# Optimization experiments

Hardware: AMD Instinct MI355X
Metric: run time of the kernel (lower is better)

The kernel has to match this reference:

```python
import jax, jax.numpy as jnp
import numpy as np

B, S, D, R = 8, 2048, 2048, 4  # batch, seq, dim, n_roles


def setup_inputs() -> dict:
    key = jax.random.key(0)
    k1, k2, k3 = jax.random.split(key, 3)
    hidden = jax.random.normal(k1, (B, S, D), dtype=jnp.float32)
    roles = jax.random.randint(k2, (B,), 0, R)
    role_onehot = jax.nn.one_hot(roles, R, dtype=jnp.float32)  # [B, R]
    # per-role Linear params (nn.Linear(dim, dim)), Kaiming-ish init scale
    W = jax.random.normal(k3, (R, D, D), dtype=jnp.float32) / np.sqrt(D)
    b = jnp.zeros((R, D), dtype=jnp.float32)
    scales = jnp.ones((R,), dtype=jnp.float32)  # role_scales
    return {"hidden": hidden, "role_onehot": role_onehot, "W": W, "b": b, "scales": scales}


def reference(hidden, role_onehot, W, b, scales):
    # Training path: compute every role's Linear+Tanh*scale, then mask-sum by one-hot.
    # transformed: [R, B, S, D]
    t = jnp.tanh(jnp.einsum('bsd,rde->rbse', hidden, W) + b[:, None, None, :])
    t = t * scales[:, None, None, None]
    # weights = role_onehot^T broadcast over (S, D); sum over roles
    return jnp.einsum('rbse,br->bse', t, role_onehot)
```

## Files before the change

kernel.cpp:

```cpp
#include <hip/hip_runtime.h>
#include <stdint.h>


#define BDIM 8
#define SDIM 2048
#define DDIM 2048
#define RDIM 4

typedef __attribute__((ext_vector_type(8))) short bf16x8;
typedef __attribute__((ext_vector_type(4))) float f32x4;

typedef unsigned int uint32;
typedef unsigned short ushort16_t;

__device__ __forceinline__ unsigned short f2bf(float f) {
    uint32 u = __float_as_uint(f);
    u += 0x7fffu + ((u >> 16) & 1u);
    return (unsigned short)(u >> 16);
}
__device__ __forceinline__ uint32 pack2(float lo, float hi) {
    return (uint32)f2bf(lo) | ((uint32)f2bf(hi) << 16);
}


__global__ __launch_bounds__(256) void cvt_h_kernel(const float* __restrict__ h,
                                                    unsigned short* __restrict__ o, int n4) {
    int i = blockIdx.x * blockDim.x + threadIdx.x;
    int stride = gridDim.x * blockDim.x;
    for (; i < n4; i += stride) {
        float4 v = reinterpret_cast<const float4*>(h)[i];
        uint2 p;
        p.x = pack2(v.x, v.y);
        p.y = pack2(v.z, v.w);
        reinterpret_cast<uint2*>(o)[i] = p;
    }
}

__global__ __launch_bounds__(256) void cvt_wt_kernel(const float* __restrict__ w,
                                                     unsigned short* __restrict__ o) {
    __shared__ unsigned short tile[32][33];
    int r = blockIdx.z;
    int e0 = blockIdx.x * 32, d0 = blockIdx.y * 32;
    const float* wr = w + (size_t)r * DDIM * DDIM;
    unsigned short* orr = o + (size_t)r * DDIM * DDIM;
    #pragma unroll
    for (int i = threadIdx.y; i < 32; i += 8)
        tile[i][threadIdx.x] = f2bf(wr[(size_t)(d0 + i) * DDIM + e0 + threadIdx.x]);
    __syncthreads();
    #pragma unroll
    for (int i = threadIdx.y; i < 32; i += 8)
        orr[(size_t)(e0 + i) * DDIM + d0 + threadIdx.x] = tile[threadIdx.x][i];
}


template <bool PRE>
__global__ __launch_bounds__(256, 2) void role_gemm(
    const void* __restrict__ Ap,
    const void* __restrict__ Bp,
    const float* __restrict__ onehot,
    const float* __restrict__ bias,
    const float* __restrict__ scales,
    float* __restrict__ out)
{
    constexpr int BK = 32;
    constexpr int NT = DDIM / BK;
    constexpr int ROWB = PRE ? (BK * 2) : (BK * 2 + 16);
    constexpr int TILEB = 128 * ROWB;
    __shared__ char lds[2 * 2 * 128 * (PRE ? 64 : 80)];

    const unsigned tid = threadIdx.x;
    const int l = tid & 63;
    const int w = tid >> 6;
    const int wm = w >> 1, wn = w & 1;
    const int fr = l & 15;
    const int fq = l >> 4;

    int bid = blockIdx.x;
    int swz = (bid & 7) * 256 + (bid >> 3);
    int batch = swz >> 8;
    int tt = swz & 255;
    int row0 = (tt >> 4) * 128;
    int n0 = (tt & 15) * 128;

    int role = 0;
    #pragma unroll
    for (int r = 1; r < RDIM; ++r) role = (onehot[batch * RDIM + r] > 0.5f) ? r : role;

    f32x4 acc[4][4];
    #pragma unroll
    for (int a = 0; a < 4; ++a)
        #pragma unroll
        for (int b2 = 0; b2 < 4; ++b2)
            #pragma unroll
            for (int r = 0; r < 4; ++r) acc[a][b2][r] = 0.0f;

    auto compute = [&](int p) {
        const char* as = lds + p * (2 * TILEB);
        const char* bs = as + TILEB;
        bf16x8 af[4], bf[4];
        #pragma unroll
        for (int a = 0; a < 4; ++a)
            af[a] = *reinterpret_cast<const bf16x8*>(as + (wm * 64 + a * 16 + fr) * ROWB + fq * 16);
        #pragma unroll
        for (int b2 = 0; b2 < 4; ++b2)
            bf[b2] = *reinterpret_cast<const bf16x8*>(bs + (wn * 64 + b2 * 16 + fr) * ROWB + fq * 16);
        #pragma unroll
        for (int a = 0; a < 4; ++a)
            #pragma unroll
            for (int b2 = 0; b2 < 4; ++b2)
                acc[a][b2] = __builtin_amdgcn_mfma_f32_16x16x32_bf16(af[a], bf[b2], acc[a][b2], 0, 0, 0);
    };

    if constexpr (PRE) {
        const unsigned short* A = (const unsigned short*)Ap + (size_t)batch * SDIM * DDIM;
        const unsigned short* Bb = (const unsigned short*)Bp + (size_t)role * DDIM * DDIM;

        auto stage = [&](int p, int k0) {
            char* as = lds + p * (2 * TILEB);
            char* bs = as + TILEB;
            #pragma unroll
            for (int j = 0; j < 2; ++j) {
                int c = j * 256 + (int)tid;
                int crow = c >> 2, ck = (c & 3) * 8;
                const unsigned short* srca = A + (size_t)(row0 + crow) * DDIM + (k0 + ck);
                char* dsta = as + (j * 256 + (int)(tid & 192)) * 16;
                __builtin_amdgcn_global_load_lds(
                    (const __attribute__((address_space(1))) void*)srca,
                    (__attribute__((address_space(3))) void*)dsta, 16, 0, 0);
                const unsigned short* srcb = Bb + (size_t)(n0 + crow) * DDIM + (k0 + ck);
                char* dstb = bs + (j * 256 + (int)(tid & 192)) * 16;
                __builtin_amdgcn_global_load_lds(
                    (const __attribute__((address_space(1))) void*)srcb,
                    (__attribute__((address_space(3))) void*)dstb, 16, 0, 0);
            }
        };

        stage(0, 0);
        __syncthreads();
        for (int t = 0; t < NT; ++t) {
            if (t + 1 < NT) stage((t + 1) & 1, (t + 1) * BK);
            compute(t & 1);
            __syncthreads();
        }
    } else {
        const float* A = (const float*)Ap + (size_t)batch * SDIM * DDIM;
        const float* Bb = (const float*)Bp + (size_t)role * DDIM * DDIM;

        const int am = (int)(tid >> 3);
        const int ak = (int)(tid & 7) * 4;
        const int bn = (int)(tid & 127);
        const int bk0 = (int)(tid >> 7) * 4;

        float4 ar[4];
        float br[16];

        auto loadregs = [&](int k0) {
            #pragma unroll
            for (int i = 0; i < 4; ++i)
                ar[i] = *reinterpret_cast<const float4*>(A + (size_t)(row0 + am + 32 * i) * DDIM + k0 + ak);
            #pragma unroll
            for (int i = 0; i < 4; ++i)
                #pragma unroll
                for (int j = 0; j < 4; ++j)
                    br[i * 4 + j] = Bb[(size_t)(k0 + bk0 + 8 * i + j) * DDIM + n0 + bn];
        };
        auto writelds = [&](int p) {
            char* as = lds + p * (2 * TILEB);
            char* bs = as + TILEB;
            #pragma unroll
            for (int i = 0; i < 4; ++i) {
                uint2 u;
                u.x = pack2(ar[i].x, ar[i].y);
                u.y = pack2(ar[i].z, ar[i].w);
                *reinterpret_cast<uint2*>(as + (am + 32 * i) * ROWB + ak * 2) = u;
            }
            #pragma unroll
            for (int i = 0; i < 4; ++i) {
                uint2 u;
                u.x = pack2(br[i * 4 + 0], br[i * 4 + 1]);
                u.y = pack2(br[i * 4 + 2], br[i * 4 + 3]);
                *reinterpret_cast<uint2*>(bs + bn * ROWB + (bk0 + 8 * i) * 2) = u;
            }
        };

        loadregs(0);
        writelds(0);
        __syncthreads();
        for (int t = 0; t < NT; ++t) {
            if (t + 1 < NT) loadregs((t + 1) * BK);
            compute(t & 1);
            if (t + 1 < NT) writelds((t + 1) & 1);
            __syncthreads();
        }
    }

    float sc = scales[role];
    const float* bp2 = bias + (size_t)role * DDIM;
    float* outb = out + ((size_t)batch * SDIM + row0) * DDIM + n0;
    #pragma unroll
    for (int a = 0; a < 4; ++a) {
        #pragma unroll
        for (int b2 = 0; b2 < 4; ++b2) {
            int col = wn * 64 + b2 * 16 + fr;
            float bb = bp2[n0 + col];
            #pragma unroll
            for (int r = 0; r < 4; ++r) {
                int row = wm * 64 + a * 16 + fq * 4 + r;
                outb[(size_t)row * DDIM + col] = tanhf(acc[a][b2][r] + bb) * sc;
            }
        }
    }
}

extern "C" void kernel_launch(void* const* d_in, const int* in_sizes, int n_in,
                              void* d_out, int out_size, void* d_ws, size_t ws_size,
                              hipStream_t stream) {
    const float* hidden = (const float*)d_in[0];
    const float* onehot = (const float*)d_in[1];
    const float* W      = (const float*)d_in[2];
    const float* bias   = (const float*)d_in[3];
    const float* scales = (const float*)d_in[4];
    float* out = (float*)d_out;

    const size_t needH = (size_t)BDIM * SDIM * DDIM * 2;
    const size_t needW = (size_t)RDIM * DDIM * DDIM * 2;

    if (d_ws != nullptr && ws_size >= needH + needW) {
        unsigned short* Hbf = (unsigned short*)d_ws;
        unsigned short* Wt  = (unsigned short*)((char*)d_ws + needH);
        cvt_h_kernel<<<2048, 256, 0, stream>>>(hidden, Hbf, BDIM * SDIM * DDIM / 4);
        cvt_wt_kernel<<<dim3(DDIM / 32, DDIM / 32, RDIM), dim3(32, 8), 0, stream>>>(W, Wt);
        role_gemm<true><<<2048, 256, 0, stream>>>(Hbf, Wt, onehot, bias, scales, out);
    } else {
        role_gemm<false><<<2048, 256, 0, stream>>>(hidden, W, onehot, bias, scales, out);
    }
}
```

Before: 468.4 us.

## Use 256x256 8-wave GEMM tile with swizzled LDS and interleaved staging

Replaces the 128x128, 4-wave bf16 GEMM with a 256x256 tile per 512-thread block, BK=64, and 128KB of dynamic LDS with an XOR-swizzled layout. Global-to-LDS staging is split into half-tiles and interleaved with quarter-tile MFMA phases using explicit waitcnt, barriers and setprio. The larger tile roughly halves global traffic per FLOP, and the swizzle is meant to avoid LDS bank conflicts. It also swaps tanhf for an exp/rcp fast tanh and widens the hidden-conversion stores to 16 bytes. The costs are heavy register pressure, a risk that 128KB LDS plus the stated two blocks per CU will not fit, and fragile hand-written synchronisation.

```diff
diff --git a/kernel.cpp b/kernel.cpp
--- a/kernel.cpp
+++ b/kernel.cpp
@@ -9,9 +9,7 @@
 
 typedef __attribute__((ext_vector_type(8))) short bf16x8;
 typedef __attribute__((ext_vector_type(4))) float f32x4;
-
 typedef unsigned int uint32;
-typedef unsigned short ushort16_t;
 
 __device__ __forceinline__ unsigned short f2bf(float f) {
     uint32 u = __float_as_uint(f);
@@ -21,18 +19,27 @@
 __device__ __forceinline__ uint32 pack2(float lo, float hi) {
     return (uint32)f2bf(lo) | ((uint32)f2bf(hi) << 16);
 }
+__device__ __forceinline__ float fast_tanh(float x) {
+    float ax = __builtin_fabsf(x);
+    float e = __expf(-2.0f * ax);
+    float t = (1.0f - e) * __builtin_amdgcn_rcpf(1.0f + e);
+    return __builtin_copysignf(t, x);
+}
 
 
 __global__ __launch_bounds__(256) void cvt_h_kernel(const float* __restrict__ h,
-                                                    unsigned short* __restrict__ o, int n4) {
+                                                    unsigned short* __restrict__ o, int n8) {
     int i = blockIdx.x * blockDim.x + threadIdx.x;
     int stride = gridDim.x * blockDim.x;
-    for (; i < n4; i += stride) {
-        float4 v = reinterpret_cast<const float4*>(h)[i];
-        uint2 p;
-        p.x = pack2(v.x, v.y);
-        p.y = pack2(v.z, v.w);
-        reinterpret_cast<uint2*>(o)[i] = p;
+    for (; i < n8; i += stride) {
+        float4 v0 = reinterpret_cast<const float4*>(h)[2 * i];
+        float4 v1 = reinterpret_cast<const float4*>(h)[2 * i + 1];
+        uint4 p;
+        p.x = pack2(v0.x, v0.y);
+        p.y = pack2(v0.z, v0.w);
+        p.z = pack2(v1.x, v1.y);
+        p.w = pack2(v1.z, v1.w);
+        reinterpret_cast<uint4*>(o)[i] = p;
     }
 }
 
@@ -53,27 +60,172 @@
 }
 
 
-template <bool PRE>
-__global__ __launch_bounds__(256, 2) void role_gemm(
-    const void* __restrict__ Ap,
-    const void* __restrict__ Bp,
+__global__ __launch_bounds__(512, 2) void role_gemm8(
+    const unsigned short* __restrict__ Hb,
+    const unsigned short* __restrict__ Wt,
     const float* __restrict__ onehot,
     const float* __restrict__ bias,
     const float* __restrict__ scales,
     float* __restrict__ out)
 {
+    constexpr int NT = DDIM / 64;
+    extern __shared__ char lds[];
+
+    const int tid = threadIdx.x;
+    const int l = tid & 63;
+    const int wv = tid >> 6;
+    const int wm = wv >> 2;
+    const int wn = wv & 3;
+    const int fr = l & 15;
+    const int fq = l >> 4;
+    const int l7 = l & 7;
+    const int colx0 = ((fq ^ l7) << 4);
+    const int colx1 = (((4 + fq) ^ l7) << 4);
+
+    int bid = blockIdx.x;
+    int swz = (bid & 7) * 64 + (bid >> 3);
+    int batch = swz >> 6;
+    int tt = swz & 63;
+    int row0 = (tt >> 3) * 256;
+    int n0 = (tt & 7) * 256;
+
+    int role = 0;
+    #pragma unroll
+    for (int r = 1; r < RDIM; ++r) role = (onehot[batch * RDIM + r] > 0.5f) ? r : role;
+
+    const unsigned short* A = Hb + (size_t)batch * SDIM * DDIM;
+    const unsigned short* Bw = Wt + (size_t)role * DDIM * DDIM;
+
+    f32x4 acc[8][4];
+    #pragma unroll
+    for (int m = 0; m < 8; ++m)
+        #pragma unroll
+        for (int n = 0; n < 4; ++n)
+            #pragma unroll
+            for (int j = 0; j < 4; ++j) acc[m][n][j] = 0.0f;
+
+    bf16x8 aR[4][2];
+    bf16x8 bQ0[2][2];
+    bf16x8 bQ1[2][2];
+
+    auto stage_half = [&](int d, int kind, int h, int T) {
+        const unsigned short* sb = kind ? Bw : A;
+        int rowbase = (kind ? n0 : row0) + h * 128;
+        char* base = lds + d * 65536 + kind * 32768 + h * 16384;
+        #pragma unroll
+        for (int j = 0; j < 2; ++j) {
+            int c = j * 512 + tid;
+            int r = c >> 3, kc = c & 7;
+            int kcs = kc ^ (r & 7);
+            const unsigned short* src = sb + (size_t)(rowbase + r) * DDIM + T * 64 + kcs * 8;
+            char* dst = base + ((j * 512 + (tid & 0x1C0)) << 4);
+            __builtin_amdgcn_global_load_lds(
+                (const __attribute__((address_space(1))) void*)src,
+                (__attribute__((address_space(3))) void*)dst, 16, 0, 0);
+        }
+    };
+
+    auto loadA = [&](int d, int mq) {
+        const char* ab = lds + d * 65536;
+        #pragma unroll
+        for (int mf = 0; mf < 4; ++mf) {
+            int rb = (wm * 128 + (mq * 4 + mf) * 16 + fr) * 128;
+            aR[mf][0] = *reinterpret_cast<const bf16x8*>(ab + rb + colx0);
+            aR[mf][1] = *reinterpret_cast<const bf16x8*>(ab + rb + colx1);
+        }
+    };
+    auto loadB = [&](int d, int nq, bf16x8 (&bR)[2][2]) {
+        const char* bb = lds + d * 65536 + 32768;
+        #pragma unroll
+        for (int nf = 0; nf < 2; ++nf) {
+            int rb = (wn * 64 + (nq * 2 + nf) * 16 + fr) * 128;
+            bR[nf][0] = *reinterpret_cast<const bf16x8*>(bb + rb + colx0);
+            bR[nf][1] = *reinterpret_cast<const bf16x8*>(bb + rb + colx1);
+        }
+    };
+    auto mmaQ = [&](int mq, int nq, bf16x8 (&bR)[2][2]) {
+        __builtin_amdgcn_s_setprio(1);
+        #pragma unroll
+        for (int mf = 0; mf < 4; ++mf)
+            #pragma unroll
+            for (int nf = 0; nf < 2; ++nf)
+                #pragma unroll
+                for (int ks = 0; ks < 2; ++ks)
+                    acc[mq * 4 + mf][nq * 2 + nf] = __builtin_amdgcn_mfma_f32_16x16x32_bf16(
+                        aR[mf][ks], bR[nf][ks], acc[mq * 4 + mf][nq * 2 + nf], 0, 0, 0);
+        __builtin_amdgcn_s_setprio(0);
+    };
+
+    stage_half(0, 1, 0, 0); stage_half(0, 1, 1, 0);
+    stage_half(0, 0, 0, 0); stage_half(0, 0, 1, 0);
+    stage_half(1, 1, 0, 1); stage_half(1, 1, 1, 1);
+    stage_half(1, 0, 0, 1);
+    asm volatile("s_waitcnt vmcnt(6)" ::: "memory");
+    __builtin_amdgcn_s_barrier();
+
+    for (int t = 0; t < NT; ++t) {
+        const int d = t & 1, e = d ^ 1;
+        loadA(d, 0);
+        loadB(d, 0, bQ0);
+        if (t + 1 < NT) stage_half(e, 0, 1, t + 1);
+        __builtin_amdgcn_s_barrier();
+        asm volatile("s_waitcnt lgkmcnt(0)" ::: "memory");
+        mmaQ(0, 0, bQ0);
+        __builtin_amdgcn_s_barrier();
+        loadB(d, 1, bQ1);
+        if (t + 2 < NT) stage_half(d, 1, 0, t + 2);
+        __builtin_amdgcn_s_barrier();
+        asm volatile("s_waitcnt lgkmcnt(0)" ::: "memory");
+        mmaQ(0, 1, bQ1);
+        __builtin_amdgcn_s_barrier();
+        loadA(d, 1);
+        if (t + 2 < NT) stage_half(d, 1, 1, t + 2);
+        __builtin_amdgcn_s_barrier();
+        asm volatile("s_waitcnt lgkmcnt(0)" ::: "memory");
+        mmaQ(1, 1, bQ1);
+        __builtin_amdgcn_s_barrier();
+        if (t + 2 < NT) stage_half(d, 0, 0, t + 2);
+        __builtin_amdgcn_s_barrier();
+        mmaQ(1, 0, bQ0);
+        if (t < NT - 2) { asm volatile("s_waitcnt vmcnt(6)" ::: "memory"); }
+        else            { asm volatile("s_waitcnt vmcnt(0)" ::: "memory"); }
+        __builtin_amdgcn_s_barrier();
+    }
+
+    float sc = scales[role];
+    const float* bp = bias + (size_t)role * DDIM;
+    float* ob = out + ((size_t)batch * SDIM + row0 + wm * 128) * DDIM + n0 + wn * 64;
+    #pragma unroll
+    for (int mfg = 0; mfg < 8; ++mfg) {
+        #pragma unroll
+        for (int nfg = 0; nfg < 4; ++nfg) {
+            int col = nfg * 16 + fr;
+            float bb = bp[n0 + wn * 64 + col];
+            #pragma unroll
+            for (int j = 0; j < 4; ++j) {
+                int row = mfg * 16 + fq * 4 + j;
+                ob[(size_t)row * DDIM + col] = fast_tanh(acc[mfg][nfg][j] + bb) * sc;
+            }
+        }
+    }
+}
+
+__global__ __launch_bounds__(256, 2) void role_gemm_fb(
+    const float* __restrict__ Ap, const float* __restrict__ Bp,
+    const float* __restrict__ onehot, const float* __restrict__ bias,
+    const float* __restrict__ scales, float* __restrict__ out)
+{
     constexpr int BK = 32;
     constexpr int NT = DDIM / BK;
-    constexpr int ROWB = PRE ? (BK * 2) : (BK * 2 + 16);
+    constexpr int ROWB = BK * 2 + 16;
     constexpr int TILEB = 128 * ROWB;
-    __shared__ char lds[2 * 2 * 128 * (PRE ? 64 : 80)];
+    __shared__ char lds[2 * 2 * 128 * 80];
 
     const unsigned tid = threadIdx.x;
     const int l = tid & 63;
     const int w = tid >> 6;
     const int wm = w >> 1, wn = w & 1;
-    const int fr = l & 15;
-    const int fq = l >> 4;
+    const int fr = l & 15, fq = l >> 4;
 
     int bid = blockIdx.x;
     int swz = (bid & 7) * 256 + (bid >> 3);
@@ -111,87 +263,52 @@
                 acc[a][b2] = __builtin_amdgcn_mfma_f32_16x16x32_bf16(af[a], bf[b2], acc[a][b2], 0, 0, 0);
     };
 
-    if constexpr (PRE) {
-        const unsigned short* A = (const unsigned short*)Ap + (size_t)batch * SDIM * DDIM;
-        const unsigned short* Bb = (const unsigned short*)Bp + (size_t)role * DDIM * DDIM;
-
-        auto stage = [&](int p, int k0) {
-            char* as = lds + p * (2 * TILEB);
-            char* bs = as + TILEB;
-            #pragma unroll
-            for (int j = 0; j < 2; ++j) {
-                int c = j * 256 + (int)tid;
-                int crow = c >> 2, ck = (c & 3) * 8;
-                const unsigned short* srca = A + (size_t)(row0 + crow) * DDIM + (k0 + ck);
-                char* dsta = as + (j * 256 + (int)(tid & 192)) * 16;
-                __builtin_amdgcn_global_load_lds(
-                    (const __attribute__((address_space(1))) void*)srca,
-                    (__attribute__((address_space(3))) void*)dsta, 16, 0, 0);
-                const unsigned short* srcb = Bb + (size_t)(n0 + crow) * DDIM + (k0 + ck);
-                char* dstb = bs + (j * 256 + (int)(tid & 192)) * 16;
-                __builtin_amdgcn_global_load_lds(
-                    (const __attribute__((address_space(1))) void*)srcb,
-                    (__attribute__((address_space(3))) void*)dstb, 16, 0, 0);
-            }
-        };
-
-        stage(0, 0);
+    const float* A = Ap + (size_t)batch * SDIM * DDIM;
+    const float* Bb = Bp + (size_t)role * DDIM * DDIM;
+    const int am = (int)(tid >> 3);
+    const int ak = (int)(tid & 7) * 4;
+    const int bn = (int)(tid & 127);
+    const int bk0 = (int)(tid >> 7) * 4;
+
+    float4 ar[4];
+    float br[16];
+    auto loadregs = [&](int k0) {
+        #pragma unroll
+        for (int i = 0; i < 4; ++i)
+            ar[i] = *reinterpret_cast<const float4*>(A + (size_t)(row0 + am + 32 * i) * DDIM + k0 + ak);
+        #pragma unroll
+        for (int i = 0; i < 4; ++i)
+            #pragma unroll
+            for (int j = 0; j < 4; ++j)
+                br[i * 4 + j] = Bb[(size_t)(k0 + bk0 + 8 * i + j) * DDIM + n0 + bn];
+    };
+    auto writelds = [&](int p) {
+        char* as = lds + p * (2 * TILEB);
+        char* bs = as + TILEB;
+        #pragma unroll
+        for (int i = 0; i < 4; ++i) {
+            uint2 u;
+            u.x = pack2(ar[i].x, ar[i].y);
+            u.y = pack2(ar[i].z, ar[i].w);
+            *reinterpret_cast<uint2*>(as + (am + 32 * i) * ROWB + ak * 2) = u;
+        }
+        #pragma unroll
+        for (int i = 0; i < 4; ++i) {
+            uint2 u;
+            u.x = pack2(br[i * 4 + 0], br[i * 4 + 1]);
+            u.y = pack2(br[i * 4 + 2], br[i * 4 + 3]);
+            *reinterpret_cast<uint2*>(bs + bn * ROWB + (bk0 + 8 * i) * 2) = u;
+        }
+    };
+
+    loadregs(0);
+    writelds(0);
+    __syncthreads();
+    for (int t = 0; t < NT; ++t) {
+        if (t + 1 < NT) loadregs((t + 1) * BK);
+        compute(t & 1);
+        if (t + 1 < NT) writelds((t + 1) & 1);
         __syncthreads();
-        for (int t = 0; t < NT; ++t) {
-            if (t + 1 < NT) stage((t + 1) & 1, (t + 1) * BK);
-            compute(t & 1);
-            __syncthreads();
-        }
-    } else {
-        const float* A = (const float*)Ap + (size_t)batch * SDIM * DDIM;
-        const float* Bb = (const float*)Bp + (size_t)role * DDIM * DDIM;
-
-        const int am = (int)(tid >> 3);
-        const int ak = (int)(tid & 7) * 4;
-        const int bn = (int)(tid & 127);
-        const int bk0 = (int)(tid >> 7) * 4;
-
-        float4 ar[4];
-        float br[16];
-
-        auto loadregs = [&](int k0) {
-            #pragma unroll
-            for (int i = 0; i < 4; ++i)
-                ar[i] = *reinterpret_cast<const float4*>(A + (size_t)(row0 + am + 32 * i) * DDIM + k0 + ak);
-            #pragma unroll
-            for (int i = 0; i < 4; ++i)
-                #pragma unroll
-                for (int j = 0; j < 4; ++j)
-                    br[i * 4 + j] = Bb[(size_t)(k0 + bk0 + 8 * i + j) * DDIM + n0 + bn];
-        };
-        auto writelds = [&](int p) {
-            char* as = lds + p * (2 * TILEB);
-            char* bs = as + TILEB;
-            #pragma unroll
-            for (int i = 0; i < 4; ++i) {
-                uint2 u;
-                u.x = pack2(ar[i].x, ar[i].y);
-                u.y = pack2(ar[i].z, ar[i].w);
-                *reinterpret_cast<uint2*>(as + (am + 32 * i) * ROWB + ak * 2) = u;
-            }
-            #pragma unroll
-            for (int i = 0; i < 4; ++i) {
-                uint2 u;
-                u.x = pack2(br[i * 4 + 0], br[i * 4 + 1]);
-                u.y = pack2(br[i * 4 + 2], br[i * 4 + 3]);
-                *reinterpret_cast<uint2*>(bs + bn * ROWB + (bk0 + 8 * i) * 2) = u;
-            }
-        };
-
-        loadregs(0);
-        writelds(0);
-        __syncthreads();
-        for (int t = 0; t < NT; ++t) {
-            if (t + 1 < NT) loadregs((t + 1) * BK);
-            compute(t & 1);
-            if (t + 1 < NT) writelds((t + 1) & 1);
-            __syncthreads();
-        }
     }
 
     float sc = scales[role];
@@ -206,7 +323,7 @@
             #pragma unroll
             for (int r = 0; r < 4; ++r) {
                 int row = wm * 64 + a * 16 + fq * 4 + r;
-                outb[(size_t)row * DDIM + col] = tanhf(acc[a][b2][r] + bb) * sc;
+                outb[(size_t)row * DDIM + col] = fast_tanh(acc[a][b2][r] + bb) * sc;
             }
         }
     }
@@ -228,10 +345,10 @@
     if (d_ws != nullptr && ws_size >= needH + needW) {
         unsigned short* Hbf = (unsigned short*)d_ws;
         unsigned short* Wt  = (unsigned short*)((char*)d_ws + needH);
-        cvt_h_kernel<<<2048, 256, 0, stream>>>(hidden, Hbf, BDIM * SDIM * DDIM / 4);
+        cvt_h_kernel<<<2048, 256, 0, stream>>>(hidden, Hbf, BDIM * SDIM * DDIM / 8);
         cvt_wt_kernel<<<dim3(DDIM / 32, DDIM / 32, RDIM), dim3(32, 8), 0, stream>>>(W, Wt);
-        role_gemm<true><<<2048, 256, 0, stream>>>(Hbf, Wt, onehot, bias, scales, out);
+        role_gemm8<<<512, 512, 131072, stream>>>(Hbf, Wt, onehot, bias, scales, out);
     } else {
-        role_gemm<false><<<2048, 256, 0, stream>>>(hidden, W, onehot, bias, scales, out);
-    }
-}
+        role_gemm_fb<<<2048, 256, 0, stream>>>(hidden, W, onehot, bias, scales, out);
+    }
+}
```

Result: faster. 404.6 us (-13.6%).
